# Optimization experiments

Measured on AMD Instinct MI355X. Metric: run time of the kernel, lower is better.

## Reference

```python
import jax, jax.numpy as jnp
import numpy as np

N = 16384          # num_nodes
B = 2              # batch_size
F = 32             # feature_size (hard-coded in module)
G = 16             # num_gru_units
OUT = 16           # output_dim


def _normalized_laplacian(adj):
    # calculate_laplacian_with_self_loop: D^-1/2 (A + I) D^-1/2
    a = adj + jnp.eye(adj.shape[0], dtype=adj.dtype)
    d = a.sum(axis=1)
    dinv = jax.lax.rsqrt(d)
    return dinv[:, None] * a * dinv[None, :]


def setup_inputs() -> dict:
    key = jax.random.key(0)
    k1, k2, k3, k4 = jax.random.split(key, 4)
    adj = (jax.random.uniform(k1, (N, N), dtype=jnp.float32) < 0.01).astype(jnp.float32)
    laplacian = _normalized_laplacian(adj)
    inputs = jax.random.normal(k2, (B, N, F), dtype=jnp.float32)
    hidden_state = jax.random.normal(k3, (B, N * G), dtype=jnp.float32)
    # xavier_uniform for weights [(G+F), OUT]
    limit = np.sqrt(6.0 / (G + F + OUT)).astype(np.float32)
    weights = jax.random.uniform(k4, (G + F, OUT), dtype=jnp.float32, minval=-limit, maxval=limit)
    biases = jnp.zeros((OUT,), dtype=jnp.float32)
    return {"inputs": inputs, "hidden_state": hidden_state, "laplacian": laplacian,
            "weights": weights, "biases": biases}


def reference(inputs, hidden_state, laplacian, weights, biases):
    b, n, f = inputs.shape
    g = weights.shape[0] - f
    out_dim = weights.shape[1]
    h = hidden_state.reshape(b, n, g)
    cat = jnp.concatenate([inputs, h], axis=2)              # [B, N, F+G]
    # laplacian @ concat over the node dimension (same math as the
    # reshape/transpose dance + per-batch sparse GEMM loop in the original)
    ax = jnp.einsum('mn,bnc->bmc', laplacian, cat)          # [B, N, F+G]
    out = ax @ weights + biases                             # [B, N, OUT]
    return out.reshape(b, n * out_dim)
```

## Files before the change

kernel.cpp:

```cpp
#include <hip/hip_runtime.h>
#include <hip/hip_bf16.h>


#define NN   16384
#define FF   32
#define GG   16
#define OUTD 16
#define C96  96
#define SPLITK 4
#define KCHUNK (NN / SPLITK)
#define KIT    (KCHUNK / 32)

typedef __attribute__((ext_vector_type(8))) short short8;
typedef __attribute__((ext_vector_type(4))) float f32x4;

__device__ __forceinline__ unsigned short f2bf(float f) {
  __hip_bfloat16 h = __float2bfloat16(f);
  return __builtin_bit_cast(unsigned short, h);
}

__global__ __launch_bounds__(256) void prep_xt(const float* __restrict__ inp,
                                               const float* __restrict__ hid,
                                               unsigned short* __restrict__ xt) {
  __shared__ float lds_cat[C96][64];
  const int tid = threadIdx.x;
  const int n0 = blockIdx.x * 64;

#pragma unroll
  for (int r = 0; r < 2; ++r) {
    int fi = tid + r * 256;
    int n = fi >> 3;
    int f4 = fi & 7;
#pragma unroll
    for (int b = 0; b < 2; ++b) {
      const float4* src = (const float4*)(inp + ((size_t)b * NN + (n0 + n)) * FF) + f4;
      float4 v = *src;
      int c = b * 48 + f4 * 4;
      lds_cat[c + 0][n] = v.x;
      lds_cat[c + 1][n] = v.y;
      lds_cat[c + 2][n] = v.z;
      lds_cat[c + 3][n] = v.w;
    }
  }
  {
    int n = tid >> 2;
    int g4 = tid & 3;
#pragma unroll
    for (int b = 0; b < 2; ++b) {
      const float4* src = (const float4*)(hid + ((size_t)b * NN + (n0 + n)) * GG) + g4;
      float4 v = *src;
      int c = b * 48 + 32 + g4 * 4;
      lds_cat[c + 0][n] = v.x;
      lds_cat[c + 1][n] = v.y;
      lds_cat[c + 2][n] = v.z;
      lds_cat[c + 3][n] = v.w;
    }
  }
  __syncthreads();
#pragma unroll
  for (int r = 0; r < 3; ++r) {
    int u = tid + r * 256;
    int c = u >> 3;
    int nn = (u & 7) * 8;
    short8 o;
#pragma unroll
    for (int j = 0; j < 8; ++j) o[j] = (short)f2bf(lds_cat[c][nn + j]);
    *(short8*)(xt + (size_t)c * NN + n0 + nn) = o;
  }
}

__global__ __launch_bounds__(256) void spmm_main(const float* __restrict__ L,
                                                 const unsigned short* __restrict__ xt,
                                                 float* __restrict__ cp) {
  const int tid = threadIdx.x;
  const int wave = tid >> 6;
  const int lane = tid & 63;
  const int m = lane & 15;
  const int quad = lane >> 4;
  const int bx = blockIdx.x;
  const int sp = bx & 3;
  const int rg = bx >> 2;
  const int m0 = rg * 128 + wave * 32;
  const int kb = sp * KCHUNK;
  const int phase = (rg * 29) & (KIT - 1);

  const float* arow0 = L + (size_t)(m0 + m) * NN + kb + quad * 8;
  const float* arow1 = arow0 + (size_t)16 * NN;
  const unsigned short* brow[6];
#pragma unroll
  for (int t = 0; t < 6; ++t)
    brow[t] = xt + (size_t)(t * 16 + m) * NN + kb + quad * 8;

  f32x4 acc[2][6];
#pragma unroll
  for (int i = 0; i < 2; ++i)
#pragma unroll
    for (int t = 0; t < 6; ++t) acc[i][t] = (f32x4){0.f, 0.f, 0.f, 0.f};

  int k0 = phase * 32;
  float4 a0n = *(const float4*)(arow0 + k0);
  float4 a1n = *(const float4*)(arow0 + k0 + 4);
  float4 a2n = *(const float4*)(arow1 + k0);
  float4 a3n = *(const float4*)(arow1 + k0 + 4);
  short8 bn[6];
#pragma unroll
  for (int t = 0; t < 6; ++t) bn[t] = *(const short8*)(brow[t] + k0);

  for (int it = 0; it < KIT; ++it) {
    float4 a0 = a0n, a1 = a1n, a2 = a2n, a3 = a3n;
    short8 bc[6];
#pragma unroll
    for (int t = 0; t < 6; ++t) bc[t] = bn[t];

    int kn = ((it + 1 + phase) & (KIT - 1)) * 32;
    a0n = *(const float4*)(arow0 + kn);
    a1n = *(const float4*)(arow0 + kn + 4);
    a2n = *(const float4*)(arow1 + kn);
    a3n = *(const float4*)(arow1 + kn + 4);
#pragma unroll
    for (int t = 0; t < 6; ++t) bn[t] = *(const short8*)(brow[t] + kn);

    short8 af0, af1;
    af0[0] = (short)f2bf(a0.x); af0[1] = (short)f2bf(a0.y);
    af0[2] = (short)f2bf(a0.z); af0[3] = (short)f2bf(a0.w);
    af0[4] = (short)f2bf(a1.x); af0[5] = (short)f2bf(a1.y);
    af0[6] = (short)f2bf(a1.z); af0[7] = (short)f2bf(a1.w);
    af1[0] = (short)f2bf(a2.x); af1[1] = (short)f2bf(a2.y);
    af1[2] = (short)f2bf(a2.z); af1[3] = (short)f2bf(a2.w);
    af1[4] = (short)f2bf(a3.x); af1[5] = (short)f2bf(a3.y);
    af1[6] = (short)f2bf(a3.z); af1[7] = (short)f2bf(a3.w);

#pragma unroll
    for (int t = 0; t < 6; ++t) {
      acc[0][t] = __builtin_amdgcn_mfma_f32_16x16x32_bf16(af0, bc[t], acc[0][t], 0, 0, 0);
      acc[1][t] = __builtin_amdgcn_mfma_f32_16x16x32_bf16(af1, bc[t], acc[1][t], 0, 0, 0);
    }
  }

  float* cpd = cp + ((size_t)sp * NN + m0) * C96;
#pragma unroll
  for (int tile = 0; tile < 2; ++tile)
#pragma unroll
    for (int t = 0; t < 6; ++t) {
      int col = t * 16 + m;
#pragma unroll
      for (int r = 0; r < 4; ++r) {
        int row = tile * 16 + quad * 4 + r;
        cpd[(size_t)row * C96 + col] = acc[tile][t][r];
      }
    }
}

__global__ __launch_bounds__(256) void epilogue(const float* __restrict__ cp,
                                                const float* __restrict__ w,
                                                const float* __restrict__ bias,
                                                float* __restrict__ out) {
  __shared__ float lds_c[64 * 97];
  __shared__ float lds_w[48 * 16];
  __shared__ float lds_bias[16];
  const int tid = threadIdx.x;
  const int n0 = blockIdx.x * 64;

  for (int i = tid; i < 768; i += 256) lds_w[i] = w[i];
  if (tid < 16) lds_bias[tid] = bias[tid];

  const size_t base = (size_t)n0 * C96;
#pragma unroll
  for (int i = 0; i < 24; ++i) {
    int e = tid + i * 256;
    float s = 0.f;
#pragma unroll
    for (int sp = 0; sp < SPLITK; ++sp)
      s += cp[(size_t)sp * ((size_t)NN * C96) + base + e];
    lds_c[e + e / 96] = s;
  }
  __syncthreads();

  const int node = tid >> 2;
  const int b = (tid >> 1) & 1;
  const int o0 = (tid & 1) * 8;
  const float* crow = &lds_c[node * 97 + b * 48];
  float accv[8];
#pragma unroll
  for (int o = 0; o < 8; ++o) accv[o] = lds_bias[o0 + o];
#pragma unroll
  for (int j = 0; j < 48; ++j) {
    float cv = crow[j];
#pragma unroll
    for (int o = 0; o < 8; ++o) accv[o] += cv * lds_w[j * 16 + o0 + o];
  }
  size_t ob = (size_t)b * ((size_t)NN * OUTD) + (size_t)(n0 + node) * OUTD + o0;
  float4 v0 = {accv[0], accv[1], accv[2], accv[3]};
  float4 v1 = {accv[4], accv[5], accv[6], accv[7]};
  *(float4*)(out + ob) = v0;
  *(float4*)(out + ob + 4) = v1;
}

extern "C" void kernel_launch(void* const* d_in, const int* in_sizes, int n_in,
                              void* d_out, int out_size, void* d_ws, size_t ws_size,
                              hipStream_t stream) {
  (void)in_sizes; (void)n_in; (void)out_size; (void)ws_size;
  const float* inp = (const float*)d_in[0];
  const float* hid = (const float*)d_in[1];
  const float* lap = (const float*)d_in[2];
  const float* wts = (const float*)d_in[3];
  const float* bia = (const float*)d_in[4];
  float* out = (float*)d_out;

  unsigned short* xt = (unsigned short*)d_ws;
  float* cp = (float*)((char*)d_ws + (4u << 20));

  prep_xt<<<NN / 64, 256, 0, stream>>>(inp, hid, xt);
  spmm_main<<<NN / 128 * SPLITK, 256, 0, stream>>>(lap, xt, cp);
  epilogue<<<NN / 64, 256, 0, stream>>>(cp, wts, bia, out);
}
```

Before: 1.443 ms.

## Replace dense MFMA GEMM with ballot-driven sparse gather over nonzero Laplacian entries

Result: faster. 1.376 ms (-4.6%).

```diff
diff --git a/kernel.cpp b/kernel.cpp
--- a/kernel.cpp
+++ b/kernel.cpp
@@ -7,148 +7,87 @@
 #define GG   16
 #define OUTD 16
 #define C96  96
-#define SPLITK 4
-#define KCHUNK (NN / SPLITK)
-#define KIT    (KCHUNK / 32)
 
-typedef __attribute__((ext_vector_type(8))) short short8;
-typedef __attribute__((ext_vector_type(4))) float f32x4;
-
-__device__ __forceinline__ unsigned short f2bf(float f) {
-  __hip_bfloat16 h = __float2bfloat16(f);
-  return __builtin_bit_cast(unsigned short, h);
+__device__ __forceinline__ unsigned int pack_bf2(float lo, float hi) {
+  unsigned short a = __builtin_bit_cast(unsigned short, __float2bfloat16(lo));
+  unsigned short b = __builtin_bit_cast(unsigned short, __float2bfloat16(hi));
+  return (unsigned int)a | ((unsigned int)b << 16);
 }
 
-__global__ __launch_bounds__(256) void prep_xt(const float* __restrict__ inp,
+__global__ __launch_bounds__(256) void prep_xp(const float* __restrict__ inp,
                                                const float* __restrict__ hid,
-                                               unsigned short* __restrict__ xt) {
-  __shared__ float lds_cat[C96][64];
-  const int tid = threadIdx.x;
-  const int n0 = blockIdx.x * 64;
+                                               unsigned int* __restrict__ xpb) {
+  int gid = blockIdx.x * 256 + threadIdx.x;
+  int k = gid / 12;
+  int j = gid - k * 12;
+  const float* src;
+  if (j < 4)       src = inp + (size_t)k * FF + 8 * j;
+  else if (j < 6)  src = hid + (size_t)k * GG + 8 * (j - 4);
+  else if (j < 10) src = inp + ((size_t)NN + k) * FF + 8 * (j - 6);
+  else             src = hid + ((size_t)NN + k) * GG + 8 * (j - 10);
+  float4 v0 = *(const float4*)src;
+  float4 v1 = *(const float4*)(src + 4);
+  uint4 o;
+  o.x = pack_bf2(v0.x, v0.y);
+  o.y = pack_bf2(v0.z, v0.w);
+  o.z = pack_bf2(v1.x, v1.y);
+  o.w = pack_bf2(v1.z, v1.w);
+  ((uint4*)xpb)[gid] = o;
+}
+
+__global__ __launch_bounds__(256) void spmm_sparse(const float* __restrict__ L,
+                                                   const unsigned int* __restrict__ xpb,
+                                                   float* __restrict__ crow) {
+  const int lane = threadIdx.x & 63;
+  const int wave = threadIdx.x >> 6;
+  const int cl = lane < 48 ? lane : lane - 48;
 
 #pragma unroll
   for (int r = 0; r < 2; ++r) {
-    int fi = tid + r * 256;
-    int n = fi >> 3;
-    int f4 = fi & 7;
+    const int m = blockIdx.x * 8 + wave * 2 + r;
+    const float4* lrow = (const float4*)(L + (size_t)m * NN);
+    float accx = 0.f, accy = 0.f;
+
+    int idx = lane * 2;
+    float4 c0 = lrow[idx];
+    float4 c1 = lrow[idx + 1];
+
+    for (int step = 0; step < 32; ++step) {
+      int nidx = (step < 31) ? idx + 128 : lane * 2;
+      float4 n0 = lrow[nidx];
+      float4 n1 = lrow[nidx + 1];
+      const int kstep = step * 512;
+
 #pragma unroll
-    for (int b = 0; b < 2; ++b) {
-      const float4* src = (const float4*)(inp + ((size_t)b * NN + (n0 + n)) * FF) + f4;
-      float4 v = *src;
-      int c = b * 48 + f4 * 4;
-      lds_cat[c + 0][n] = v.x;
-      lds_cat[c + 1][n] = v.y;
-      lds_cat[c + 2][n] = v.z;
-      lds_cat[c + 3][n] = v.w;
+      for (int s = 0; s < 8; ++s) {
+        float v;
+        switch (s) {
+          case 0: v = c0.x; break; case 1: v = c0.y; break;
+          case 2: v = c0.z; break; case 3: v = c0.w; break;
+          case 4: v = c1.x; break; case 5: v = c1.y; break;
+          case 6: v = c1.z; break; default: v = c1.w; break;
+        }
+        unsigned long long msk = __ballot(v != 0.0f);
+        while (msk) {
+          int b = __builtin_ctzll(msk);
+          msk &= msk - 1;
+          float val = __shfl(v, b);
+          int k = kstep + 8 * b + s;
+          unsigned int u = xpb[(size_t)k * 48 + cl];
+          float x0 = __builtin_bit_cast(float, u << 16);
+          float x1 = __builtin_bit_cast(float, u & 0xffff0000u);
+          accx += val * x0;
+          accy += val * x1;
+        }
+      }
+      c0 = n0; c1 = n1; idx = nidx;
+    }
+
+    if (lane < 48) {
+      float2 o = {accx, accy};
+      *(float2*)(crow + (size_t)m * C96 + 2 * lane) = o;
     }
   }
-  {
-    int n = tid >> 2;
-    int g4 = tid & 3;
-#pragma unroll
-    for (int b = 0; b < 2; ++b) {
-      const float4* src = (const float4*)(hid + ((size_t)b * NN + (n0 + n)) * GG) + g4;
-      float4 v = *src;
-      int c = b * 48 + 32 + g4 * 4;
-      lds_cat[c + 0][n] = v.x;
-      lds_cat[c + 1][n] = v.y;
-      lds_cat[c + 2][n] = v.z;
-      lds_cat[c + 3][n] = v.w;
-    }
-  }
-  __syncthreads();
-#pragma unroll
-  for (int r = 0; r < 3; ++r) {
-    int u = tid + r * 256;
-    int c = u >> 3;
-    int nn = (u & 7) * 8;
-    short8 o;
-#pragma unroll
-    for (int j = 0; j < 8; ++j) o[j] = (short)f2bf(lds_cat[c][nn + j]);
-    *(short8*)(xt + (size_t)c * NN + n0 + nn) = o;
-  }
-}
-
-__global__ __launch_bounds__(256) void spmm_main(const float* __restrict__ L,
-                                                 const unsigned short* __restrict__ xt,
-                                                 float* __restrict__ cp) {
-  const int tid = threadIdx.x;
-  const int wave = tid >> 6;
-  const int lane = tid & 63;
-  const int m = lane & 15;
-  const int quad = lane >> 4;
-  const int bx = blockIdx.x;
-  const int sp = bx & 3;
-  const int rg = bx >> 2;
-  const int m0 = rg * 128 + wave * 32;
-  const int kb = sp * KCHUNK;
-  const int phase = (rg * 29) & (KIT - 1);
-
-  const float* arow0 = L + (size_t)(m0 + m) * NN + kb + quad * 8;
-  const float* arow1 = arow0 + (size_t)16 * NN;
-  const unsigned short* brow[6];
-#pragma unroll
-  for (int t = 0; t < 6; ++t)
-    brow[t] = xt + (size_t)(t * 16 + m) * NN + kb + quad * 8;
-
-  f32x4 acc[2][6];
-#pragma unroll
-  for (int i = 0; i < 2; ++i)
-#pragma unroll
-    for (int t = 0; t < 6; ++t) acc[i][t] = (f32x4){0.f, 0.f, 0.f, 0.f};
-
-  int k0 = phase * 32;
-  float4 a0n = *(const float4*)(arow0 + k0);
-  float4 a1n = *(const float4*)(arow0 + k0 + 4);
-  float4 a2n = *(const float4*)(arow1 + k0);
-  float4 a3n = *(const float4*)(arow1 + k0 + 4);
-  short8 bn[6];
-#pragma unroll
-  for (int t = 0; t < 6; ++t) bn[t] = *(const short8*)(brow[t] + k0);
-
-  for (int it = 0; it < KIT; ++it) {
-    float4 a0 = a0n, a1 = a1n, a2 = a2n, a3 = a3n;
-    short8 bc[6];
-#pragma unroll
-    for (int t = 0; t < 6; ++t) bc[t] = bn[t];
-
-    int kn = ((it + 1 + phase) & (KIT - 1)) * 32;
-    a0n = *(const float4*)(arow0 + kn);
-    a1n = *(const float4*)(arow0 + kn + 4);
-    a2n = *(const float4*)(arow1 + kn);
-    a3n = *(const float4*)(arow1 + kn + 4);
-#pragma unroll
-    for (int t = 0; t < 6; ++t) bn[t] = *(const short8*)(brow[t] + kn);
-
-    short8 af0, af1;
-    af0[0] = (short)f2bf(a0.x); af0[1] = (short)f2bf(a0.y);
-    af0[2] = (short)f2bf(a0.z); af0[3] = (short)f2bf(a0.w);
-    af0[4] = (short)f2bf(a1.x); af0[5] = (short)f2bf(a1.y);
-    af0[6] = (short)f2bf(a1.z); af0[7] = (short)f2bf(a1.w);
-    af1[0] = (short)f2bf(a2.x); af1[1] = (short)f2bf(a2.y);
-    af1[2] = (short)f2bf(a2.z); af1[3] = (short)f2bf(a2.w);
-    af1[4] = (short)f2bf(a3.x); af1[5] = (short)f2bf(a3.y);
-    af1[6] = (short)f2bf(a3.z); af1[7] = (short)f2bf(a3.w);
-
-#pragma unroll
-    for (int t = 0; t < 6; ++t) {
-      acc[0][t] = __builtin_amdgcn_mfma_f32_16x16x32_bf16(af0, bc[t], acc[0][t], 0, 0, 0);
-      acc[1][t] = __builtin_amdgcn_mfma_f32_16x16x32_bf16(af1, bc[t], acc[1][t], 0, 0, 0);
-    }
-  }
-
-  float* cpd = cp + ((size_t)sp * NN + m0) * C96;
-#pragma unroll
-  for (int tile = 0; tile < 2; ++tile)
-#pragma unroll
-    for (int t = 0; t < 6; ++t) {
-      int col = t * 16 + m;
-#pragma unroll
-      for (int r = 0; r < 4; ++r) {
-        int row = tile * 16 + quad * 4 + r;
-        cpd[(size_t)row * C96 + col] = acc[tile][t][r];
-      }
-    }
 }
 
 __global__ __launch_bounds__(256) void epilogue(const float* __restrict__ cp,
@@ -168,24 +107,20 @@
 #pragma unroll
   for (int i = 0; i < 24; ++i) {
     int e = tid + i * 256;
-    float s = 0.f;
-#pragma unroll
-    for (int sp = 0; sp < SPLITK; ++sp)
-      s += cp[(size_t)sp * ((size_t)NN * C96) + base + e];
-    lds_c[e + e / 96] = s;
+    lds_c[e + e / 96] = cp[base + e];
   }
   __syncthreads();
 
   const int node = tid >> 2;
   const int b = (tid >> 1) & 1;
   const int o0 = (tid & 1) * 8;
-  const float* crow = &lds_c[node * 97 + b * 48];
+  const float* crow_l = &lds_c[node * 97 + b * 48];
   float accv[8];
 #pragma unroll
   for (int o = 0; o < 8; ++o) accv[o] = lds_bias[o0 + o];
 #pragma unroll
   for (int j = 0; j < 48; ++j) {
-    float cv = crow[j];
+    float cv = crow_l[j];
 #pragma unroll
     for (int o = 0; o < 8; ++o) accv[o] += cv * lds_w[j * 16 + o0 + o];
   }
@@ -207,10 +142,10 @@
   const float* bia = (const float*)d_in[4];
   float* out = (float*)d_out;
 
-  unsigned short* xt = (unsigned short*)d_ws;
-  float* cp = (float*)((char*)d_ws + (4u << 20));
+  unsigned int* xpb = (unsigned int*)d_ws;
+  float* crow = (float*)((char*)d_ws + (4u << 20));
 
-  prep_xt<<<NN / 64, 256, 0, stream>>>(inp, hid, xt);
-  spmm_main<<<NN / 128 * SPLITK, 256, 0, stream>>>(lap, xt, cp);
-  epilogue<<<NN / 64, 256, 0, stream>>>(cp, wts, bia, out);
+  prep_xp<<<(NN * 12) / 256, 256, 0, stream>>>(inp, hid, xpb);
+  spmm_sparse<<<NN / 8, 256, 0, stream>>>(lap, xpb, crow);
+  epilogue<<<NN / 64, 256, 0, stream>>>(crow, wts, bia, out);
 }
```
